# Kernel tuning notes

Hardware: AMD Instinct MI355X
Metric: run time of the kernel (lower is better)

The kernel has to match this reference:

```python
import jax, jax.numpy as jnp
import numpy as np

EMBED_DIM = 512
NUM_HEADS = 8
HEAD_DIM = EMBED_DIM // NUM_HEADS
EDGE_DIM = 16
B, N = 2, 2048


def setup_inputs() -> dict:
    key = jax.random.key(0)
    ks = jax.random.split(key, 16)
    s = 1.0 / np.sqrt(EMBED_DIM)
    inp = {
        "x": jax.random.normal(ks[0], (B, N, EMBED_DIM), dtype=jnp.float32),
        "adjacency": jax.random.uniform(ks[1], (B, N, N), dtype=jnp.float32),
        # torch.nn.Linear stores weight as (out, in); we keep that convention
        "Wq": jax.random.uniform(ks[2], (EMBED_DIM, EMBED_DIM), minval=-s, maxval=s),
        "bq": jax.random.uniform(ks[3], (EMBED_DIM,), minval=-s, maxval=s),
        "Wk": jax.random.uniform(ks[4], (EMBED_DIM, EMBED_DIM), minval=-s, maxval=s),
        "bk": jax.random.uniform(ks[5], (EMBED_DIM,), minval=-s, maxval=s),
        "Wv": jax.random.uniform(ks[6], (EMBED_DIM, EMBED_DIM), minval=-s, maxval=s),
        "bv": jax.random.uniform(ks[7], (EMBED_DIM,), minval=-s, maxval=s),
        "Wo": jax.random.uniform(ks[8], (EMBED_DIM, EMBED_DIM), minval=-s, maxval=s),
        "bo": jax.random.uniform(ks[9], (EMBED_DIM,), minval=-s, maxval=s),
        # edge MLP: Linear(1 -> edge_dim) then Linear(edge_dim -> num_heads)
        "We1": jax.random.uniform(ks[10], (EDGE_DIM, 1), minval=-1.0, maxval=1.0),
        "be1": jax.random.uniform(ks[11], (EDGE_DIM,), minval=-1.0, maxval=1.0),
        "We2": jax.random.uniform(ks[12], (NUM_HEADS, EDGE_DIM), minval=-0.25, maxval=0.25),
        "be2": jax.random.uniform(ks[13], (NUM_HEADS,), minval=-0.25, maxval=0.25),
        "edge_bias": jnp.zeros((NUM_HEADS,), dtype=jnp.float32),
    }
    return inp


def reference(x, adjacency, Wq, bq, Wk, bk, Wv, bv, Wo, bo, We1, be1, We2, be2, edge_bias):
    b, n, _ = x.shape
    scale = HEAD_DIM ** (-0.5)

    def split_heads(t):  # (b, n, E) -> (b, H, n, d)
        return t.reshape(b, n, NUM_HEADS, HEAD_DIM).transpose(0, 2, 1, 3)

    q = split_heads(x @ Wq.T + bq)
    k = split_heads(x @ Wk.T + bk)
    v = split_heads(x @ Wv.T + bv)

    # (b, H, n, n)
    attn_scores = jnp.einsum('bhid,bhjd->bhij', q, k) * scale

    # edge MLP applied pointwise to each adjacency entry: 1 -> edge_dim -> num_heads
    # hidden: (b, n, n, edge_dim)
    hidden = jax.nn.relu(adjacency[..., None] * We1[:, 0] + be1)
    edge_attn = jnp.einsum('bijE,hE->bhij', hidden, We2) + be2[None, :, None, None]

    boost = adjacency[:, None, :, :] * edge_bias[None, :, None, None]
    attn_scores = attn_scores + edge_attn + boost

    attn_probs = jax.nn.softmax(attn_scores, axis=-1)
    out = jnp.einsum('bhij,bhjd->bhid', attn_probs, v)
    out = out.transpose(0, 2, 1, 3).reshape(b, n, EMBED_DIM)
    out = out @ Wo.T + bo
    return out
```

## Files before the change

### kernel.cpp

```cpp
#include <hip/hip_runtime.h>
#include <stdint.h>


#define SEQ 2048
#define EMB 512
#define NH  8
#define HD  64
#define NB  2

typedef unsigned int   u32;
typedef unsigned short u16;
typedef u32   u32x4  __attribute__((ext_vector_type(4)));
typedef float f32x4  __attribute__((ext_vector_type(4)));
typedef __bf16 bf16x8 __attribute__((ext_vector_type(8)));

#define MFMA16(a, b, c) __builtin_amdgcn_mfma_f32_16x16x32_bf16((a), (b), (c), 0, 0, 0)

static __device__ __forceinline__ u16 f2bf(float f) {
  u32 u = __builtin_bit_cast(u32, f);
  return (u16)((u + 0x7fffu + ((u >> 16) & 1u)) >> 16);
}
static __device__ __forceinline__ bf16x8 ldfrag(const u16* p) {
  return __builtin_bit_cast(bf16x8, *(const u32x4*)p);
}

__global__ void cvt_bf16_kernel(const float* __restrict__ s, u16* __restrict__ d, int n) {
  int i = (blockIdx.x * blockDim.x + threadIdx.x) * 4;
  if (i >= n) return;
  float4 v = *(const float4*)(s + i);
  u32 lo = (u32)f2bf(v.x) | ((u32)f2bf(v.y) << 16);
  u32 hi = (u32)f2bf(v.z) | ((u32)f2bf(v.w) << 16);
  *(uint2*)(d + i) = make_uint2(lo, hi);
}

__global__ void edge_coeff_kernel(const float* __restrict__ We1, const float* __restrict__ be1,
                                  const float* __restrict__ We2, const float* __restrict__ be2,
                                  const float* __restrict__ ebias, float* __restrict__ co) {
  if (threadIdx.x != 0 || blockIdx.x != 0) return;
  float A[NH], Bc[NH];
  for (int h = 0; h < NH; h++) { A[h] = be2[h]; Bc[h] = ebias[h]; }
  int m = 0;
  for (int e = 0; e < 16; e++) {
    float w1 = We1[e], b1 = be1[e];
    float u0 = b1, u1 = w1 + b1;
    if (u0 >= 0.0f && u1 >= 0.0f) {
      for (int h = 0; h < NH; h++) { float w2 = We2[h*16+e]; A[h] += w2*b1; Bc[h] += w2*w1; }
    } else if (u0 <= 0.0f && u1 <= 0.0f) {
    } else {
      for (int h = 0; h < NH; h++) {
        float w2 = We2[h*16+e];
        A[h]  += 0.5f*w2*b1;
        Bc[h] += 0.5f*w2*w1;
        co[49 + m*8 + h] = 0.5f*w2;
      }
      co[17+m] = w1; co[33+m] = b1; m++;
    }
  }
  for (int h = 0; h < NH; h++) { co[h] = A[h]; co[8+h] = Bc[h]; }
  ((int*)co)[16] = m;
}

#define LDA 40
__global__ __launch_bounds__(256) void gemm_qkv_kernel(
    const u16* __restrict__ A, const u16* __restrict__ Bm,
    const float* __restrict__ bq, const float* __restrict__ bk, const float* __restrict__ bv,
    u16* __restrict__ qh, u16* __restrict__ kh, u16* __restrict__ vh)
{
  __shared__ u16 As[128 * LDA];
  __shared__ u16 Bs[128 * LDA];
  const int tid = threadIdx.x;
  const int lane = tid & 63, wid = tid >> 6;
  const int q = lane >> 4, l15 = lane & 15;
  const int m0 = blockIdx.y * 128;
  const int n0 = blockIdx.x * 128;
  const int wh = wid >> 1, ww = wid & 1;

  f32x4 acc[4][4];
  f32x4 zero = {0.f, 0.f, 0.f, 0.f};
  #pragma unroll
  for (int i = 0; i < 4; i++)
    #pragma unroll
    for (int j = 0; j < 4; j++) acc[i][j] = zero;

  const int srow = tid >> 1, shalf = tid & 1;
  const u16* ga = A  + (size_t)(m0 + srow) * EMB + shalf * 16;
  const u16* gb = Bm + (size_t)(n0 + srow) * EMB + shalf * 16;
  u16* la = &As[srow * LDA + shalf * 16];
  u16* lb = &Bs[srow * LDA + shalf * 16];

  for (int k0 = 0; k0 < EMB; k0 += 32) {
    __syncthreads();
    u32x4 a0 = *(const u32x4*)(ga);
    u32x4 a1 = *(const u32x4*)(ga + 8);
    u32x4 b0 = *(const u32x4*)(gb);
    u32x4 b1 = *(const u32x4*)(gb + 8);
    ga += 32; gb += 32;
    *(u32x4*)(la)     = a0; *(u32x4*)(la + 8) = a1;
    *(u32x4*)(lb)     = b0; *(u32x4*)(lb + 8) = b1;
    __syncthreads();
    bf16x8 af[4], bfr[4];
    #pragma unroll
    for (int mi = 0; mi < 4; mi++)
      af[mi] = ldfrag(&As[(wh*64 + mi*16 + l15) * LDA + q*8]);
    #pragma unroll
    for (int ni = 0; ni < 4; ni++)
      bfr[ni] = ldfrag(&Bs[(ww*64 + ni*16 + l15) * LDA + q*8]);
    #pragma unroll
    for (int mi = 0; mi < 4; mi++)
      #pragma unroll
      for (int ni = 0; ni < 4; ni++)
        acc[mi][ni] = MFMA16(af[mi], bfr[ni], acc[mi][ni]);
  }

  const int mat = n0 >> 9;
  const float* bias = (mat == 0) ? bq : ((mat == 1) ? bk : bv);
  u16* dst = (mat == 0) ? qh : ((mat == 1) ? kh : vh);
  const float mul = (mat == 0) ? 0.125f : 1.0f;

  #pragma unroll
  for (int mi = 0; mi < 4; mi++) {
    int rowb = m0 + wh*64 + mi*16 + q*4;
    #pragma unroll
    for (int ni = 0; ni < 4; ni++) {
      int col = n0 + ww*64 + ni*16 + l15;
      int oo = col & 511;
      float bsv = bias[oo];
      int h = oo >> 6, dd = oo & 63;
      #pragma unroll
      for (int r = 0; r < 4; r++) {
        int grow = rowb + r;
        int b_ = grow >> 11, n_ = grow & 2047;
        float val = (acc[mi][ni][r] + bsv) * mul;
        dst[((size_t)(b_ * NH + h) * SEQ + n_) * HD + dd] = f2bf(val);
      }
    }
  }
}

__global__ __launch_bounds__(256) void gemm_out_kernel(
    const u16* __restrict__ A, const u16* __restrict__ Bm,
    const float* __restrict__ bo, float* __restrict__ out)
{
  __shared__ u16 As[128 * LDA];
  __shared__ u16 Bs[128 * LDA];
  const int tid = threadIdx.x;
  const int lane = tid & 63, wid = tid >> 6;
  const int q = lane >> 4, l15 = lane & 15;
  const int m0 = blockIdx.y * 128;
  const int n0 = blockIdx.x * 128;
  const int wh = wid >> 1, ww = wid & 1;

  f32x4 acc[4][4];
  f32x4 zero = {0.f, 0.f, 0.f, 0.f};
  #pragma unroll
  for (int i = 0; i < 4; i++)
    #pragma unroll
    for (int j = 0; j < 4; j++) acc[i][j] = zero;

  const int srow = tid >> 1, shalf = tid & 1;
  const u16* ga = A  + (size_t)(m0 + srow) * EMB + shalf * 16;
  const u16* gb = Bm + (size_t)(n0 + srow) * EMB + shalf * 16;
  u16* la = &As[srow * LDA + shalf * 16];
  u16* lb = &Bs[srow * LDA + shalf * 16];

  for (int k0 = 0; k0 < EMB; k0 += 32) {
    __syncthreads();
    u32x4 a0 = *(const u32x4*)(ga);
    u32x4 a1 = *(const u32x4*)(ga + 8);
    u32x4 b0 = *(const u32x4*)(gb);
    u32x4 b1 = *(const u32x4*)(gb + 8);
    ga += 32; gb += 32;
    *(u32x4*)(la)     = a0; *(u32x4*)(la + 8) = a1;
    *(u32x4*)(lb)     = b0; *(u32x4*)(lb + 8) = b1;
    __syncthreads();
    bf16x8 af[4], bfr[4];
    #pragma unroll
    for (int mi = 0; mi < 4; mi++)
      af[mi] = ldfrag(&As[(wh*64 + mi*16 + l15) * LDA + q*8]);
    #pragma unroll
    for (int ni = 0; ni < 4; ni++)
      bfr[ni] = ldfrag(&Bs[(ww*64 + ni*16 + l15) * LDA + q*8]);
    #pragma unroll
    for (int mi = 0; mi < 4; mi++)
      #pragma unroll
      for (int ni = 0; ni < 4; ni++)
        acc[mi][ni] = MFMA16(af[mi], bfr[ni], acc[mi][ni]);
  }

  #pragma unroll
  for (int mi = 0; mi < 4; mi++) {
    int rowb = m0 + wh*64 + mi*16 + q*4;
    #pragma unroll
    for (int ni = 0; ni < 4; ni++) {
      int col = n0 + ww*64 + ni*16 + l15;
      float bsv = bo[col];
      #pragma unroll
      for (int r = 0; r < 4; r++)
        out[(size_t)(rowb + r) * EMB + col] = acc[mi][ni][r] + bsv;
    }
  }
}

__global__ __launch_bounds__(256) void vtrans_kernel(const u16* __restrict__ vh, u16* __restrict__ vt) {
  __shared__ u16 Ts[64 * 72];
  const int b = blockIdx.z, h = blockIdx.y, j0 = blockIdx.x * 64;
  const int t = threadIdx.x;
  const u16* src = vh + ((size_t)(b * NH + h) * SEQ + j0) * HD;
  {
    int r = t >> 2, c = t & 3;
    *(u32x4*)&Ts[r*72 + c*16]     = *(const u32x4*)(src + r*HD + c*16);
    *(u32x4*)&Ts[r*72 + c*16 + 8] = *(const u32x4*)(src + r*HD + c*16 + 8);
  }
  __syncthreads();
  int d = t >> 2, jc = t & 3;
  u32 w[8];
  #pragma unroll
  for (int p = 0; p < 8; p++) {
    u32 lo = Ts[(jc*16 + 2*p    ) * 72 + d];
    u32 hi = Ts[(jc*16 + 2*p + 1) * 72 + d];
    w[p] = lo | (hi << 16);
  }
  u16* dst = vt + ((size_t)(b * NH + h) * HD + d) * SEQ + j0 + jc * 16;
  u32x4 w0 = {w[0], w[1], w[2], w[3]};
  u32x4 w1 = {w[4], w[5], w[6], w[7]};
  *(u32x4*)(dst)     = w0;
  *(u32x4*)(dst + 8) = w1;
}

__global__ __launch_bounds__(256) void flash_kernel(
    const u16* __restrict__ qh, const u16* __restrict__ kh, const u16* __restrict__ vt,
    const float* __restrict__ adj, const float* __restrict__ coeff, u16* __restrict__ om)
{
  __shared__ u16 Ks[64 * 72];
  __shared__ u16 Vs[64 * 72];
  __shared__ u16 Ps[4 * 16 * 72];
  __shared__ u16 Os[64 * 72];
  __shared__ float l_lds[4][16];

  const int tid = threadIdx.x, lane = tid & 63, w = tid >> 6;
  const int q = lane >> 4, l15 = lane & 15;
  const int i0 = blockIdx.x * 64;
  const int h = blockIdx.y, b = blockIdx.z;
  const int bh = b * NH + h;

  const float Ah = coeff[h], Bh = coeff[8 + h];
  const int mterms = ((const int*)coeff)[16];

  const u16* qbase = qh + ((size_t)bh * SEQ + i0 + w*16 + l15) * HD + q*8;
  bf16x8 qf0 = ldfrag(qbase);
  bf16x8 qf1 = ldfrag(qbase + 32);

  f32x4 O[4];
  f32x4 zero = {0.f, 0.f, 0.f, 0.f};
  #pragma unroll
  for (int dt = 0; dt < 4; dt++) O[dt] = zero;
  float lsum[4] = {0.f, 0.f, 0.f, 0.f};

  const u16* kgbase = kh + (size_t)bh * SEQ * HD;
  const u16* vgbase = vt + (size_t)bh * HD * SEQ;
  const float* abase = adj + ((size_t)b * SEQ + i0 + w*16 + q*4) * SEQ;

  const int sr = tid >> 2, sc = tid & 3;
  u16* psw = &Ps[w * 16 * 72];

  for (int jc = 0; jc < SEQ; jc += 64) {
    __syncthreads();
    {
      const u16* g = kgbase + (size_t)(jc + sr) * HD + sc * 16;
      u32x4 v0 = *(const u32x4*)g;
      u32x4 v1 = *(const u32x4*)(g + 8);
      *(u32x4*)&Ks[sr*72 + sc*16]     = v0;
      *(u32x4*)&Ks[sr*72 + sc*16 + 8] = v1;
      const u16* g2 = vgbase + (size_t)sr * SEQ + jc + sc * 16;
      u32x4 u0 = *(const u32x4*)g2;
      u32x4 u1 = *(const u32x4*)(g2 + 8);
      *(u32x4*)&Vs[sr*72 + sc*16]     = u0;
      *(u32x4*)&Vs[sr*72 + sc*16 + 8] = u1;
    }
    __syncthreads();

    float av[4][4];
    #pragma unroll
    for (int jt = 0; jt < 4; jt++)
      #pragma unroll
      for (int r = 0; r < 4; r++)
        av[jt][r] = abase[(size_t)r * SEQ + jc + jt*16 + l15];

    f32x4 S[4];
    #pragma unroll
    for (int jt = 0; jt < 4; jt++) {
      bf16x8 kf0 = ldfrag(&Ks[(jt*16 + l15) * 72 + q*8]);
      bf16x8 kf1 = ldfrag(&Ks[(jt*16 + l15) * 72 + 32 + q*8]);
      f32x4 s = zero;
      s = MFMA16(qf0, kf0, s);
      s = MFMA16(qf1, kf1, s);
      S[jt] = s;
    }

    float eb[4][4];
    #pragma unroll
    for (int jt = 0; jt < 4; jt++)
      #pragma unroll
      for (int r = 0; r < 4; r++)
        eb[jt][r] = fmaf(av[jt][r], Bh, Ah);
    for (int t = 0; t < mterms; t++) {
      float ct = coeff[17 + t], dt_ = coeff[33 + t], wt = coeff[49 + t*8 + h];
      #pragma unroll
      for (int jt = 0; jt < 4; jt++)
        #pragma unroll
        for (int r = 0; r < 4; r++)
          eb[jt][r] = fmaf(fabsf(fmaf(av[jt][r], ct, dt_)), wt, eb[jt][r]);
    }

    #pragma unroll
    for (int jt = 0; jt < 4; jt++) {
      #pragma unroll
      for (int r = 0; r < 4; r++) {
        float p = __expf(S[jt][r] + eb[jt][r]);
        lsum[r] += p;
        psw[(q*4 + r) * 72 + jt*16 + l15] = f2bf(p);
      }
    }

    bf16x8 pf0 = ldfrag(&psw[l15 * 72 + q*8]);
    bf16x8 pf1 = ldfrag(&psw[l15 * 72 + 32 + q*8]);
    #pragma unroll
    for (int dt = 0; dt < 4; dt++) {
      bf16x8 vf0 = ldfrag(&Vs[(dt*16 + l15) * 72 + q*8]);
      bf16x8 vf1 = ldfrag(&Vs[(dt*16 + l15) * 72 + 32 + q*8]);
      O[dt] = MFMA16(vf0, pf0, O[dt]);
      O[dt] = MFMA16(vf1, pf1, O[dt]);
    }
  }

  #pragma unroll
  for (int r = 0; r < 4; r++) {
    float v = lsum[r];
    v += __shfl_xor(v, 1);
    v += __shfl_xor(v, 2);
    v += __shfl_xor(v, 4);
    v += __shfl_xor(v, 8);
    l_lds[w][q*4 + r] = v;
  }
  float rl = 1.0f / l_lds[w][l15];

  #pragma unroll
  for (int dt = 0; dt < 4; dt++)
    #pragma unroll
    for (int r = 0; r < 4; r++)
      Os[(w*16 + l15) * 72 + dt*16 + q*4 + r] = f2bf(O[dt][r] * rl);
  __syncthreads();
  {
    int orow = tid >> 2, oc = tid & 3;
    u32x4 o0 = *(const u32x4*)&Os[orow*72 + oc*16];
    u32x4 o1 = *(const u32x4*)&Os[orow*72 + oc*16 + 8];
    u16* dst = om + ((size_t)b * SEQ + i0 + orow) * EMB + h * HD + oc * 16;
    *(u32x4*)(dst)     = o0;
    *(u32x4*)(dst + 8) = o1;
  }
}

extern "C" void kernel_launch(void* const* d_in, const int* in_sizes, int n_in,
                              void* d_out, int out_size, void* d_ws, size_t ws_size,
                              hipStream_t stream) {
  const float* x     = (const float*)d_in[0];
  const float* adj   = (const float*)d_in[1];
  const float* Wq    = (const float*)d_in[2];
  const float* bq    = (const float*)d_in[3];
  const float* Wk    = (const float*)d_in[4];
  const float* bk    = (const float*)d_in[5];
  const float* Wv    = (const float*)d_in[6];
  const float* bv    = (const float*)d_in[7];
  const float* Wo    = (const float*)d_in[8];
  const float* bo    = (const float*)d_in[9];
  const float* We1   = (const float*)d_in[10];
  const float* be1   = (const float*)d_in[11];
  const float* We2   = (const float*)d_in[12];
  const float* be2   = (const float*)d_in[13];
  const float* ebias = (const float*)d_in[14];
  float* out = (float*)d_out;

  char* ws = (char*)d_ws;
  u16*   xb   = (u16*)(ws + 0);
  u16*   wqkv = (u16*)(ws + 4194304);
  u16*   wob  = (u16*)(ws + 5767168);
  u16*   qh   = (u16*)(ws + 6291456);
  u16*   kh   = (u16*)(ws + 10485760);
  u16*   vh   = (u16*)(ws + 14680064);
  u16*   vt   = (u16*)(ws + 18874368);
  u16*   om   = (u16*)(ws + 23068672);
  float* co   = (float*)(ws + 27262976);
  if (ws_size < 27264000) return;

  cvt_bf16_kernel<<<2048, 256, 0, stream>>>(x, xb, NB * SEQ * EMB);
  cvt_bf16_kernel<<<256, 256, 0, stream>>>(Wq, wqkv + 0 * EMB * EMB, EMB * EMB);
  cvt_bf16_kernel<<<256, 256, 0, stream>>>(Wk, wqkv + 1 * EMB * EMB, EMB * EMB);
  cvt_bf16_kernel<<<256, 256, 0, stream>>>(Wv, wqkv + 2 * EMB * EMB, EMB * EMB);
  cvt_bf16_kernel<<<256, 256, 0, stream>>>(Wo, wob, EMB * EMB);
  edge_coeff_kernel<<<1, 64, 0, stream>>>(We1, be1, We2, be2, ebias, co);
  gemm_qkv_kernel<<<dim3(12, 32), 256, 0, stream>>>(xb, wqkv, bq, bk, bv, qh, kh, vh);
  vtrans_kernel<<<dim3(32, NH, NB), 256, 0, stream>>>(vh, vt);
  flash_kernel<<<dim3(32, NH, NB), 256, 0, stream>>>(qh, kh, vt, adj, co, om);
  gemm_out_kernel<<<dim3(4, 32), 256, 0, stream>>>(om, wob, bo, out);
}
```

Baseline: 214.0 us.

## Prefetch next tiles in GEMMs and flash loop, merge weight casts, parallelize edge coeffs

Adds register prefetch of the next K/V and adjacency tiles in the flash kernel and of the next A/B tiles in both GEMMs, so global loads overlap with compute. The four weight-cast launches become one kernel, and the edge-coefficient setup runs across 128 threads using shuffles and a ballot instead of a single thread. The output GEMM moves to 64-row tiles so more blocks launch, and the flash epilogue writes straight to global memory instead of staging in LDS, with the MFMA operand order swapped to match. This raises register pressure, and the direct epilogue stores are less coalesced.

```diff
diff --git a/kernel.cpp b/kernel.cpp
--- a/kernel.cpp
+++ b/kernel.cpp
@@ -33,31 +33,47 @@
   *(uint2*)(d + i) = make_uint2(lo, hi);
 }
 
+__global__ void cvt_w_kernel(const float* __restrict__ Wq, const float* __restrict__ Wk,
+                             const float* __restrict__ Wv, const float* __restrict__ Wo,
+                             u16* __restrict__ wqkv, u16* __restrict__ wob) {
+  int i = (blockIdx.x * blockDim.x + threadIdx.x) * 4;
+  int m = i >> 18;
+  int off = i & 262143;
+  const float* src = (m == 0) ? Wq : ((m == 1) ? Wk : ((m == 2) ? Wv : Wo));
+  u16* dst = (m < 3) ? (wqkv + (size_t)m * 262144) : wob;
+  float4 v = *(const float4*)(src + off);
+  u32 lo = (u32)f2bf(v.x) | ((u32)f2bf(v.y) << 16);
+  u32 hi = (u32)f2bf(v.z) | ((u32)f2bf(v.w) << 16);
+  *(uint2*)(dst + off) = make_uint2(lo, hi);
+}
+
 __global__ void edge_coeff_kernel(const float* __restrict__ We1, const float* __restrict__ be1,
                                   const float* __restrict__ We2, const float* __restrict__ be2,
                                   const float* __restrict__ ebias, float* __restrict__ co) {
-  if (threadIdx.x != 0 || blockIdx.x != 0) return;
-  float A[NH], Bc[NH];
-  for (int h = 0; h < NH; h++) { A[h] = be2[h]; Bc[h] = ebias[h]; }
-  int m = 0;
-  for (int e = 0; e < 16; e++) {
-    float w1 = We1[e], b1 = be1[e];
-    float u0 = b1, u1 = w1 + b1;
-    if (u0 >= 0.0f && u1 >= 0.0f) {
-      for (int h = 0; h < NH; h++) { float w2 = We2[h*16+e]; A[h] += w2*b1; Bc[h] += w2*w1; }
-    } else if (u0 <= 0.0f && u1 <= 0.0f) {
-    } else {
-      for (int h = 0; h < NH; h++) {
-        float w2 = We2[h*16+e];
-        A[h]  += 0.5f*w2*b1;
-        Bc[h] += 0.5f*w2*w1;
-        co[49 + m*8 + h] = 0.5f*w2;
-      }
-      co[17+m] = w1; co[33+m] = b1; m++;
-    }
-  }
-  for (int h = 0; h < NH; h++) { co[h] = A[h]; co[8+h] = Bc[h]; }
-  ((int*)co)[16] = m;
+  const int t = threadIdx.x;
+  const int e = t & 15, h = t >> 4;
+  float w1 = We1[e], b1 = be1[e], w2 = We2[h * 16 + e];
+  float u0 = b1, u1 = w1 + b1;
+  bool on  = (u0 >= 0.0f) && (u1 >= 0.0f);
+  bool off = (u0 <= 0.0f) && (u1 <= 0.0f);
+  bool crossing = (!on) && (!off);
+  float ca = on ? (w2 * b1) : (crossing ? 0.5f * w2 * b1 : 0.0f);
+  float cb = on ? (w2 * w1) : (crossing ? 0.5f * w2 * w1 : 0.0f);
+  #pragma unroll
+  for (int d = 1; d < 16; d <<= 1) {
+    ca += __shfl_xor(ca, d);
+    cb += __shfl_xor(cb, d);
+  }
+  if (e == 0) { co[h] = be2[h] + ca; co[8 + h] = ebias[h] + cb; }
+  unsigned long long msk = __ballot(crossing);
+  int midx = __popcll(msk & 0xFFFFull & ((1ull << e) - 1ull));
+  int mcnt = __popcll(msk & 0xFFFFull);
+  if (crossing) {
+    co[49 + midx * 8 + h] = 0.5f * w2;
+    if (h == 0 || h == 4) {  }
+    if (h == 0) { co[17 + midx] = w1; co[33 + midx] = b1; }
+  }
+  if (t == 0) ((int*)co)[16] = mcnt;
 }
 
 #define LDA 40
@@ -88,16 +104,24 @@
   u16* la = &As[srow * LDA + shalf * 16];
   u16* lb = &Bs[srow * LDA + shalf * 16];
 
+  u32x4 pa0 = *(const u32x4*)(ga);
+  u32x4 pa1 = *(const u32x4*)(ga + 8);
+  u32x4 pb0 = *(const u32x4*)(gb);
+  u32x4 pb1 = *(const u32x4*)(gb + 8);
+  ga += 32; gb += 32;
+
   for (int k0 = 0; k0 < EMB; k0 += 32) {
     __syncthreads();
-    u32x4 a0 = *(const u32x4*)(ga);
-    u32x4 a1 = *(const u32x4*)(ga + 8);
-    u32x4 b0 = *(const u32x4*)(gb);
-    u32x4 b1 = *(const u32x4*)(gb + 8);
-    ga += 32; gb += 32;
-    *(u32x4*)(la)     = a0; *(u32x4*)(la + 8) = a1;
-    *(u32x4*)(lb)     = b0; *(u32x4*)(lb + 8) = b1;
-    __syncthreads();
+    *(u32x4*)(la)     = pa0; *(u32x4*)(la + 8) = pa1;
+    *(u32x4*)(lb)     = pb0; *(u32x4*)(lb + 8) = pb1;
+    __syncthreads();
+    if (k0 + 32 < EMB) {
+      pa0 = *(const u32x4*)(ga);
+      pa1 = *(const u32x4*)(ga + 8);
+      pb0 = *(const u32x4*)(gb);
+      pb1 = *(const u32x4*)(gb + 8);
+      ga += 32; gb += 32;
+    }
     bf16x8 af[4], bfr[4];
     #pragma unroll
     for (int mi = 0; mi < 4; mi++)
@@ -141,58 +165,82 @@
     const u16* __restrict__ A, const u16* __restrict__ Bm,
     const float* __restrict__ bo, float* __restrict__ out)
 {
-  __shared__ u16 As[128 * LDA];
+  __shared__ u16 As[64 * LDA];
   __shared__ u16 Bs[128 * LDA];
   const int tid = threadIdx.x;
-  const int lane = tid & 63, wid = tid >> 6;
+  const int lane = tid & 63, w = tid >> 6;
   const int q = lane >> 4, l15 = lane & 15;
-  const int m0 = blockIdx.y * 128;
+  const int m0 = blockIdx.y * 64;
   const int n0 = blockIdx.x * 128;
-  const int wh = wid >> 1, ww = wid & 1;
-
-  f32x4 acc[4][4];
+
+  f32x4 acc[4][2];
   f32x4 zero = {0.f, 0.f, 0.f, 0.f};
   #pragma unroll
-  for (int i = 0; i < 4; i++)
-    #pragma unroll
-    for (int j = 0; j < 4; j++) acc[i][j] = zero;
-
-  const int srow = tid >> 1, shalf = tid & 1;
-  const u16* ga = A  + (size_t)(m0 + srow) * EMB + shalf * 16;
-  const u16* gb = Bm + (size_t)(n0 + srow) * EMB + shalf * 16;
-  u16* la = &As[srow * LDA + shalf * 16];
-  u16* lb = &Bs[srow * LDA + shalf * 16];
+  for (int i = 0; i < 4; i++) { acc[i][0] = zero; acc[i][1] = zero; }
+
+  const bool isA = tid < 128;
+  const int arow = tid >> 1, ahalf = tid & 1;
+  const int brow = tid - 128;
+  const u16* ga = A  + (size_t)(m0 + arow) * EMB + ahalf * 16;
+  const u16* gb = Bm + (size_t)(n0 + brow) * EMB;
+  u16* la = &As[arow * LDA + ahalf * 16];
+  u16* lb = &Bs[brow * LDA];
+
+  u32x4 p0, p1, p2, p3;
+  if (isA) {
+    p0 = *(const u32x4*)(ga);
+    p1 = *(const u32x4*)(ga + 8);
+    ga += 32;
+  } else {
+    p0 = *(const u32x4*)(gb);
+    p1 = *(const u32x4*)(gb + 8);
+    p2 = *(const u32x4*)(gb + 16);
+    p3 = *(const u32x4*)(gb + 24);
+    gb += 32;
+  }
 
   for (int k0 = 0; k0 < EMB; k0 += 32) {
     __syncthreads();
-    u32x4 a0 = *(const u32x4*)(ga);
-    u32x4 a1 = *(const u32x4*)(ga + 8);
-    u32x4 b0 = *(const u32x4*)(gb);
-    u32x4 b1 = *(const u32x4*)(gb + 8);
-    ga += 32; gb += 32;
-    *(u32x4*)(la)     = a0; *(u32x4*)(la + 8) = a1;
-    *(u32x4*)(lb)     = b0; *(u32x4*)(lb + 8) = b1;
-    __syncthreads();
-    bf16x8 af[4], bfr[4];
+    if (isA) {
+      *(u32x4*)(la)     = p0; *(u32x4*)(la + 8) = p1;
+    } else {
+      *(u32x4*)(lb)      = p0; *(u32x4*)(lb + 8)  = p1;
+      *(u32x4*)(lb + 16) = p2; *(u32x4*)(lb + 24) = p3;
+    }
+    __syncthreads();
+    if (k0 + 32 < EMB) {
+      if (isA) {
+        p0 = *(const u32x4*)(ga);
+        p1 = *(const u32x4*)(ga + 8);
+        ga += 32;
+      } else {
+        p0 = *(const u32x4*)(gb);
+        p1 = *(const u32x4*)(gb + 8);
+        p2 = *(const u32x4*)(gb + 16);
+        p3 = *(const u32x4*)(gb + 24);
+        gb += 32;
+      }
+    }
+    bf16x8 af[4], bfr[2];
     #pragma unroll
     for (int mi = 0; mi < 4; mi++)
-      af[mi] = ldfrag(&As[(wh*64 + mi*16 + l15) * LDA + q*8]);
-    #pragma unroll
-    for (int ni = 0; ni < 4; ni++)
-      bfr[ni] = ldfrag(&Bs[(ww*64 + ni*16 + l15) * LDA + q*8]);
+      af[mi] = ldfrag(&As[(mi*16 + l15) * LDA + q*8]);
+    #pragma unroll
+    for (int ni = 0; ni < 2; ni++)
+      bfr[ni] = ldfrag(&Bs[(w*32 + ni*16 + l15) * LDA + q*8]);
     #pragma unroll
     for (int mi = 0; mi < 4; mi++)
       #pragma unroll
-      for (int ni = 0; ni < 4; ni++)
+      for (int ni = 0; ni < 2; ni++)
         acc[mi][ni] = MFMA16(af[mi], bfr[ni], acc[mi][ni]);
   }
 
   #pragma unroll
   for (int mi = 0; mi < 4; mi++) {
-    int rowb = m0 + wh*64 + mi*16 + q*4;
-    #pragma unroll
-    for (int ni = 0; ni < 4; ni++) {
-      int col = n0 + ww*64 + ni*16 + l15;
+    int rowb = m0 + mi*16 + q*4;
+    #pragma unroll
+    for (int ni = 0; ni < 2; ni++) {
+      int col = n0 + w*32 + ni*16 + l15;
       float bsv = bo[col];
       #pragma unroll
       for (int r = 0; r < 4; r++)
@@ -213,16 +261,16 @@
   }
   __syncthreads();
   int d = t >> 2, jc = t & 3;
-  u32 w[8];
+  u32 wv[8];
   #pragma unroll
   for (int p = 0; p < 8; p++) {
     u32 lo = Ts[(jc*16 + 2*p    ) * 72 + d];
     u32 hi = Ts[(jc*16 + 2*p + 1) * 72 + d];
-    w[p] = lo | (hi << 16);
+    wv[p] = lo | (hi << 16);
   }
   u16* dst = vt + ((size_t)(b * NH + h) * HD + d) * SEQ + j0 + jc * 16;
-  u32x4 w0 = {w[0], w[1], w[2], w[3]};
-  u32x4 w1 = {w[4], w[5], w[6], w[7]};
+  u32x4 w0 = {wv[0], wv[1], wv[2], wv[3]};
+  u32x4 w1 = {wv[4], wv[5], wv[6], wv[7]};
   *(u32x4*)(dst)     = w0;
   *(u32x4*)(dst + 8) = w1;
 }
@@ -234,8 +282,6 @@
   __shared__ u16 Ks[64 * 72];
   __shared__ u16 Vs[64 * 72];
   __shared__ u16 Ps[4 * 16 * 72];
-  __shared__ u16 Os[64 * 72];
-  __shared__ float l_lds[4][16];
 
   const int tid = threadIdx.x, lane = tid & 63, w = tid >> 6;
   const int q = lane >> 4, l15 = lane & 15;
@@ -263,28 +309,61 @@
   const int sr = tid >> 2, sc = tid & 3;
   u16* psw = &Ps[w * 16 * 72];
 
-  for (int jc = 0; jc < SEQ; jc += 64) {
-    __syncthreads();
+  u32x4 pk0, pk1, pv0, pv1;
+  float padj[16];
+  {
+    const u16* gk = kgbase + (size_t)sr * HD + sc * 16;
+    const u16* gv = vgbase + (size_t)sr * SEQ + sc * 16;
+    pk0 = *(const u32x4*)(gk);
+    pk1 = *(const u32x4*)(gk + 8);
+    pv0 = *(const u32x4*)(gv);
+    pv1 = *(const u32x4*)(gv + 8);
+    #pragma unroll
+    for (int jt = 0; jt < 4; jt++)
+      #pragma unroll
+      for (int r = 0; r < 4; r++)
+        padj[jt*4 + r] = abase[(size_t)r * SEQ + jt*16 + l15];
+  }
+
+  for (int it = 0; it < 32; it++) {
+    __syncthreads();
+    *(u32x4*)&Ks[sr*72 + sc*16]     = pk0;
+    *(u32x4*)&Ks[sr*72 + sc*16 + 8] = pk1;
+    *(u32x4*)&Vs[sr*72 + sc*16]     = pv0;
+    *(u32x4*)&Vs[sr*72 + sc*16 + 8] = pv1;
+    __syncthreads();
+
+    const int nx = (it + 1 < 32) ? (it + 1) * 64 : 0;
+
     {
-      const u16* g = kgbase + (size_t)(jc + sr) * HD + sc * 16;
-      u32x4 v0 = *(const u32x4*)g;
-      u32x4 v1 = *(const u32x4*)(g + 8);
-      *(u32x4*)&Ks[sr*72 + sc*16]     = v0;
-      *(u32x4*)&Ks[sr*72 + sc*16 + 8] = v1;
-      const u16* g2 = vgbase + (size_t)sr * SEQ + jc + sc * 16;
-      u32x4 u0 = *(const u32x4*)g2;
-      u32x4 u1 = *(const u32x4*)(g2 + 8);
-      *(u32x4*)&Vs[sr*72 + sc*16]     = u0;
-      *(u32x4*)&Vs[sr*72 + sc*16 + 8] = u1;
-    }
-    __syncthreads();
-
-    float av[4][4];
+      const u16* gk = kgbase + (size_t)(nx + sr) * HD + sc * 16;
+      const u16* gv = vgbase + (size_t)sr * SEQ + nx + sc * 16;
+      pk0 = *(const u32x4*)(gk);
+      pk1 = *(const u32x4*)(gk + 8);
+      pv0 = *(const u32x4*)(gv);
+      pv1 = *(const u32x4*)(gv + 8);
+    }
+
+    float eb[16];
     #pragma unroll
     for (int jt = 0; jt < 4; jt++)
       #pragma unroll
       for (int r = 0; r < 4; r++)
-        av[jt][r] = abase[(size_t)r * SEQ + jc + jt*16 + l15];
+        eb[jt*4 + r] = fmaf(padj[jt*4 + r], Bh, Ah);
+    for (int t = 0; t < mterms; t++) {
+      float ct = coeff[17 + t], dt_ = coeff[33 + t], wt = coeff[49 + t*8 + h];
+      #pragma unroll
+      for (int jt = 0; jt < 4; jt++)
+        #pragma unroll
+        for (int r = 0; r < 4; r++)
+          eb[jt*4 + r] = fmaf(fabsf(fmaf(padj[jt*4 + r], ct, dt_)), wt, eb[jt*4 + r]);
+    }
+
+    #pragma unroll
+    for (int jt = 0; jt < 4; jt++)
+      #pragma unroll
+      for (int r = 0; r < 4; r++)
+        padj[jt*4 + r] = abase[(size_t)r * SEQ + nx + jt*16 + l15];
 
     f32x4 S[4];
     #pragma unroll
@@ -297,26 +376,11 @@
       S[jt] = s;
     }
 
-    float eb[4][4];
-    #pragma unroll
-    for (int jt = 0; jt < 4; jt++)
-      #pragma unroll
-      for (int r = 0; r < 4; r++)
-        eb[jt][r] = fmaf(av[jt][r], Bh, Ah);
-    for (int t = 0; t < mterms; t++) {
-      float ct = coeff[17 + t], dt_ = coeff[33 + t], wt = coeff[49 + t*8 + h];
-      #pragma unroll
-      for (int jt = 0; jt < 4; jt++)
-        #pragma unroll
-        for (int r = 0; r < 4; r++)
-          eb[jt][r] = fmaf(fabsf(fmaf(av[jt][r], ct, dt_)), wt, eb[jt][r]);
-    }
-
     #pragma unroll
     for (int jt = 0; jt < 4; jt++) {
       #pragma unroll
       for (int r = 0; r < 4; r++) {
-        float p = __expf(S[jt][r] + eb[jt][r]);
+        float p = __expf(S[jt][r] + eb[jt*4 + r]);
         lsum[r] += p;
         psw[(q*4 + r) * 72 + jt*16 + l15] = f2bf(p);
       }
@@ -328,11 +392,12 @@
     for (int dt = 0; dt < 4; dt++) {
       bf16x8 vf0 = ldfrag(&Vs[(dt*16 + l15) * 72 + q*8]);
       bf16x8 vf1 = ldfrag(&Vs[(dt*16 + l15) * 72 + 32 + q*8]);
-      O[dt] = MFMA16(vf0, pf0, O[dt]);
-      O[dt] = MFMA16(vf1, pf1, O[dt]);
-    }
-  }
-
+      O[dt] = MFMA16(pf0, vf0, O[dt]);
+      O[dt] = MFMA16(pf1, vf1, O[dt]);
+    }
+  }
+
+  float rl[4];
   #pragma unroll
   for (int r = 0; r < 4; r++) {
     float v = lsum[r];
@@ -340,24 +405,15 @@
     v += __shfl_xor(v, 2);
     v += __shfl_xor(v, 4);
     v += __shfl_xor(v, 8);
-    l_lds[w][q*4 + r] = v;
-  }
-  float rl = 1.0f / l_lds[w][l15];
+    rl[r] = 1.0f / v;
+  }
 
   #pragma unroll
   for (int dt = 0; dt < 4; dt++)
     #pragma unroll
     for (int r = 0; r < 4; r++)
-      Os[(w*16 + l15) * 72 + dt*16 + q*4 + r] = f2bf(O[dt][r] * rl);
-  __syncthreads();
-  {
-    int orow = tid >> 2, oc = tid & 3;
-    u32x4 o0 = *(const u32x4*)&Os[orow*72 + oc*16];
-    u32x4 o1 = *(const u32x4*)&Os[orow*72 + oc*16 + 8];
-    u16* dst = om + ((size_t)b * SEQ + i0 + orow) * EMB + h * HD + oc * 16;
-    *(u32x4*)(dst)     = o0;
-    *(u32x4*)(dst + 8) = o1;
-  }
+      om[((size_t)b * SEQ + i0 + w*16 + q*4 + r) * EMB + h * HD + dt*16 + l15] =
+          f2bf(O[dt][r] * rl[r]);
 }
 
 extern "C" void kernel_launch(void* const* d_in, const int* in_sizes, int n_in,
@@ -393,13 +449,10 @@
   if (ws_size < 27264000) return;
 
   cvt_bf16_kernel<<<2048, 256, 0, stream>>>(x, xb, NB * SEQ * EMB);
-  cvt_bf16_kernel<<<256, 256, 0, stream>>>(Wq, wqkv + 0 * EMB * EMB, EMB * EMB);
-  cvt_bf16_kernel<<<256, 256, 0, stream>>>(Wk, wqkv + 1 * EMB * EMB, EMB * EMB);
-  cvt_bf16_kernel<<<256, 256, 0, stream>>>(Wv, wqkv + 2 * EMB * EMB, EMB * EMB);
-  cvt_bf16_kernel<<<256, 256, 0, stream>>>(Wo, wob, EMB * EMB);
-  edge_coeff_kernel<<<1, 64, 0, stream>>>(We1, be1, We2, be2, ebias, co);
+  cvt_w_kernel<<<1024, 256, 0, stream>>>(Wq, Wk, Wv, Wo, wqkv, wob);
+  edge_coeff_kernel<<<1, 128, 0, stream>>>(We1, be1, We2, be2, ebias, co);
   gemm_qkv_kernel<<<dim3(12, 32), 256, 0, stream>>>(xb, wqkv, bq, bk, bv, qh, kh, vh);
   vtrans_kernel<<<dim3(32, NH, NB), 256, 0, stream>>>(vh, vt);
   flash_kernel<<<dim3(32, NH, NB), 256, 0, stream>>>(qh, kh, vt, adj, co, om);
-  gemm_out_kernel<<<dim3(4, 32), 256, 0, stream>>>(om, wob, bo, out);
-}
+  gemm_out_kernel<<<dim3(4, 64), 256, 0, stream>>>(om, wob, bo, out);
+}
```

Result: faster. 199.7 us (-6.7%).
